# Kernel optimization log

Measured on AMD Instinct MI355X. Metric: run time of the kernel, lower is better.

Reference implementation:

```python
import math
import jax, jax.numpy as jnp
import numpy as np

B, LD, LS = 1, 512, 2048
C_S, C_H, H, PQ, PV = 384, 16, 12, 4, 8
EPS, INF = 1e-08, 1e9


def _quat_to_rot(q):
    q = q / jnp.linalg.norm(q, axis=-1, keepdims=True)
    w, x, y, z = q[..., 0], q[..., 1], q[..., 2], q[..., 3]
    R = jnp.stack([
        1 - 2 * (y * y + z * z), 2 * (x * y - w * z), 2 * (x * z + w * y),
        2 * (x * y + w * z), 1 - 2 * (x * x + z * z), 2 * (y * z - w * x),
        2 * (x * z - w * y), 2 * (y * z + w * x), 1 - 2 * (x * x + y * y)],
        axis=-1)
    return R.reshape(q.shape[:-1] + (3, 3))


def setup_inputs() -> dict:
    key = jax.random.key(0)
    ks = jax.random.split(key, 14)
    s_dst = jax.random.normal(ks[0], (B, LD, C_S), jnp.float32)
    s_src = jax.random.normal(ks[1], (B, LS, C_S), jnp.float32)
    R_dst = _quat_to_rot(jax.random.normal(ks[2], (B, LD, 4), jnp.float32))
    t_dst = jax.random.normal(ks[3], (B, LD, 3), jnp.float32) * 3.0
    R_src = _quat_to_rot(jax.random.normal(ks[4], (B, LS, 4), jnp.float32))
    t_src = jax.random.normal(ks[5], (B, LS, 3), jnp.float32) * 3.0
    dst_mask = jnp.ones((B, LD), jnp.float32)
    src_mask = (jax.random.uniform(ks[6], (B, LS)) < 0.9).astype(jnp.float32)
    sc = 0.02
    W_q = jax.random.normal(ks[7], (C_S, H * C_H), jnp.float32) * sc
    W_kv = jax.random.normal(ks[8], (C_S, 2 * H * C_H), jnp.float32) * sc
    W_qp = jax.random.normal(ks[9], (C_S, H * PQ * 3), jnp.float32) * sc
    W_kvp = jax.random.normal(ks[10], (C_S, H * (PQ + PV) * 3), jnp.float32) * sc
    W_out = jax.random.normal(ks[11], (H * (C_H + PV * 4), C_S), jnp.float32) * sc
    b_out = jnp.zeros((C_S,), jnp.float32)
    # ipa_point_weights_init_: softplus^-1(1) = log(e - 1)
    head_w = jnp.full((H,), float(np.log(np.e - 1.0)), jnp.float32)
    return dict(s_dst=s_dst, s_src=s_src, R_dst=R_dst, t_dst=t_dst,
                R_src=R_src, t_src=t_src, dst_mask=dst_mask, src_mask=src_mask,
                W_q=W_q, W_kv=W_kv, W_qp=W_qp, W_kvp=W_kvp,
                W_out=W_out, b_out=b_out, head_w=head_w)


def _split3_stack(x):
    # torch.split into 3 chunks on last dim then stack(dim=-1): [..., 3n] -> [..., n, 3]
    b, l, c3 = x.shape
    return jnp.moveaxis(x.reshape(b, l, 3, c3 // 3), -2, -1)


def _ipa_forward(s_dst, s_src, R_dst, t_dst, R_src, t_src, dst_mask, src_mask,
                 W_q, W_kv, W_qp, W_kvp, W_out, b_out, head_w):
    b, ld, _ = s_dst.shape
    ls = s_src.shape[1]
    gmask = (dst_mask[:, None, :, None] * src_mask[:, None, None, :])  # [B,1,Ld,Ls]

    q = (s_dst @ W_q).reshape(b, ld, H, C_H)
    kv = (s_src @ W_kv).reshape(b, ls, H, 2 * C_H)
    k, v = kv[..., :C_H], kv[..., C_H:]

    # points in global frame
    qp = _split3_stack(s_dst @ W_qp)                     # [B,Ld,H*PQ,3] local
    qp = jnp.einsum('blij,blpj->blpi', R_dst, qp) + t_dst[:, :, None, :]
    qp = qp.reshape(b, ld, H, PQ, 3)
    kvp = _split3_stack(s_src @ W_kvp)                   # [B,Ls,H*(PQ+PV),3]
    kvp = jnp.einsum('blij,blpj->blpi', R_src, kvp) + t_src[:, :, None, :]
    kvp = kvp.reshape(b, ls, H, PQ + PV, 3)
    k_pts, v_pts = kvp[..., :PQ, :], kvp[..., PQ:, :]

    # scalar attention scores
    a = jnp.einsum('bihc,bjhc->bhij', q, k) * math.sqrt(1.0 / (2 * C_H))
    a_sd = a * gmask

    # point attention: squared distances of global-frame points
    diff = qp[:, :, None, :, :, :] - k_pts[:, None, :, :, :, :]   # [B,Ld,Ls,H,PQ,3]
    pt2 = jnp.sum(diff * diff, axis=-1)                           # [B,Ld,Ls,H,PQ]
    hw = jax.nn.softplus(head_w) * math.sqrt(1.0 / (2 * (PQ * 9.0 / 2)))
    pt_att = jnp.sum(pt2 * hw[None, None, None, :, None], axis=-1) * (-0.5)
    pt_att = jnp.transpose(pt_att, (0, 3, 1, 2))                  # [B,H,Ld,Ls]
    a_pts = pt_att * gmask

    sq_mask = INF * (dst_mask[:, :, None] * src_mask[:, None, :] - 1.0)
    a = jax.nn.softmax(a + pt_att + sq_mask[:, None, :, :], axis=-1)

    # scalar value aggregation
    o = jnp.einsum('bhij,bjhc->bihc', a, v).reshape(b, ld, H * C_H)
    # point value aggregation, then back to dst local frame
    o_pt = jnp.einsum('bhij,bjhpc->bihpc', a, v_pts)              # [B,Ld,H,PV,3]
    o_pt = jnp.einsum('bikj,bihpk->bihpj', R_dst,
                      o_pt - t_dst[:, :, None, None, :])
    o_pt_norm = jnp.sqrt(jnp.sum(o_pt ** 2, axis=-1) + EPS).reshape(b, ld, H * PV)
    o_pt_flat = o_pt.reshape(b, ld, H * PV, 3)

    cat = jnp.concatenate([o, o_pt_flat[..., 0], o_pt_flat[..., 1],
                           o_pt_flat[..., 2], o_pt_norm], axis=-1)
    s_upd = cat @ W_out + b_out
    return s_upd, a, a_sd, a_pts


def reference(s_dst, s_src, R_dst, t_dst, R_src, t_src, dst_mask, src_mask,
              W_q, W_kv, W_qp, W_kvp, W_out, b_out, head_w):
    return _ipa_forward(s_dst, s_src, R_dst, t_dst, R_src, t_src,
                        dst_mask, src_mask, W_q, W_kv, W_qp, W_kvp,
                        W_out, b_out, head_w)
```

## Files before the change

### kernel.cpp

```cpp
#include <hip/hip_runtime.h>
#include <hip/hip_bf16.h>

#define LD 512
#define LS 2048
#define CS 384
#define CH 16
#define NH 12
#define PQ 4
#define PV 8
#define QCW 336
#define KVW 816

typedef __bf16 bf16x8 __attribute__((ext_vector_type(8)));
typedef float  f32x4  __attribute__((ext_vector_type(4)));

__device__ inline bf16x8 conv_frag(const float* __restrict__ p)
{
    float4 x = *(const float4*)p;
    float4 y = *(const float4*)(p + 4);
    bf16x8 h;
    h[0] = (__bf16)x.x; h[1] = (__bf16)x.y; h[2] = (__bf16)x.z; h[3] = (__bf16)x.w;
    h[4] = (__bf16)y.x; h[5] = (__bf16)y.y; h[6] = (__bf16)y.z; h[7] = (__bf16)y.w;
    return h;
}

__device__ inline bf16x8 conv_frag_w(const float* __restrict__ Wp, int stride)
{
    float f[8];
#pragma unroll
    for (int e = 0; e < 8; ++e) f[e] = Wp[(size_t)e * stride];
    bf16x8 h;
#pragma unroll
    for (int e = 0; e < 8; ++e) h[e] = (__bf16)f[e];
    return h;
}

__global__ __launch_bounds__(64) void proj_gemm_kernel(
    const float* __restrict__ s_dst, const float* __restrict__ s_src,
    const float* __restrict__ W_q, const float* __restrict__ W_qp,
    const float* __restrict__ W_kv, const float* __restrict__ W_kvp,
    float* __restrict__ qcat, float* __restrict__ kvcat)
{
    const float* A; float* C; int N, m0, n0, Nw; const float* Wsrc; int ncol0;
    if (blockIdx.x < 176) {
        int b = blockIdx.x;
        A = s_dst; C = qcat; N = QCW;
        m0 = (b & 15) * 32; n0 = (b >> 4) * 32;
        if (n0 < 192) { Wsrc = W_q;  Nw = 192; ncol0 = n0; }
        else          { Wsrc = W_qp; Nw = 144; ncol0 = n0 - 192; }
    } else {
        int b = blockIdx.x - 176;
        A = s_src; C = kvcat; N = KVW;
        m0 = (b & 63) * 32; n0 = (b >> 6) * 32;
        if (n0 < 384) { Wsrc = W_kv;  Nw = 384; ncol0 = n0; }
        else          { Wsrc = W_kvp; Nw = 432; ncol0 = n0 - 384; }
    }
    const int lane = threadIdx.x;
    const int row16 = lane & 15, kq = lane >> 4;
    const int K = CS;

    const float* ap0 = A + (size_t)(m0 + row16) * K + kq * 8;
    const float* ap1 = ap0 + (size_t)16 * K;
    const float* wp0 = Wsrc + (size_t)(kq * 8) * Nw + ncol0 + row16;
    const float* wp1 = wp0 + 16;
    const bool n1ok = (n0 + 16) < N;

    f32x4 acc00 = {0.f, 0.f, 0.f, 0.f};
    f32x4 acc10 = {0.f, 0.f, 0.f, 0.f};
    f32x4 acc01 = {0.f, 0.f, 0.f, 0.f};
    f32x4 acc11 = {0.f, 0.f, 0.f, 0.f};

    for (int k = 0; k < K; k += 32) {
        bf16x8 a0 = conv_frag(ap0 + k);
        bf16x8 a1 = conv_frag(ap1 + k);
        bf16x8 b0 = conv_frag_w(wp0 + (size_t)k * Nw, Nw);
        acc00 = __builtin_amdgcn_mfma_f32_16x16x32_bf16(a0, b0, acc00, 0, 0, 0);
        acc10 = __builtin_amdgcn_mfma_f32_16x16x32_bf16(a1, b0, acc10, 0, 0, 0);
        if (n1ok) {
            bf16x8 b1 = conv_frag_w(wp1 + (size_t)k * Nw, Nw);
            acc01 = __builtin_amdgcn_mfma_f32_16x16x32_bf16(a0, b1, acc01, 0, 0, 0);
            acc11 = __builtin_amdgcn_mfma_f32_16x16x32_bf16(a1, b1, acc11, 0, 0, 0);
        }
    }

#pragma unroll
    for (int r = 0; r < 4; ++r) {
        const int mA = m0 + kq * 4 + r;
        const int mB = mA + 16;
        C[(size_t)mA * N + n0 + row16] = acc00[r];
        C[(size_t)mB * N + n0 + row16] = acc10[r];
        if (n1ok) {
            C[(size_t)mA * N + n0 + 16 + row16] = acc01[r];
            C[(size_t)mB * N + n0 + 16 + row16] = acc11[r];
        }
    }
}

__global__ __launch_bounds__(256) void prep_kernel(
    const float* __restrict__ qcat, const float* __restrict__ kvcat,
    const float* __restrict__ Rd, const float* __restrict__ td,
    const float* __restrict__ Rs, const float* __restrict__ ts,
    float* __restrict__ qp_rot, float* __restrict__ sqq,
    float* __restrict__ kT, float* __restrict__ vAllT,
    float* __restrict__ kpT, float* __restrict__ sqkT)
{
    const int t = threadIdx.x;
    if (blockIdx.y < NH) {
        const int h = blockIdx.y, j0 = blockIdx.x * 64;
        __shared__ float tile[64][33];
        __shared__ float ot[36][64];
        __shared__ float nrm[64][4];
        __shared__ float rt[64][12];

#pragma unroll
        for (int s = 0; s < 3; ++s) {
            int ld = t + s * 256;
            int jl = ld / 12, q = ld % 12;
            rt[jl][q] = (q < 9) ? Rs[(size_t)(j0 + jl) * 9 + q]
                                : ts[(size_t)(j0 + jl) * 3 + (q - 9)];
        }
#pragma unroll
        for (int r = 0; r < 2; ++r) {
            int f = t + r * 256;
            int jl = f >> 3, c4 = (f & 7) * 4;
            float4 v = *(const float4*)(kvcat + (size_t)(j0 + jl) * KVW + h * 32 + c4);
            tile[jl][c4 + 0] = v.x;
            tile[jl][c4 + 1] = v.y;
            tile[jl][c4 + 2] = v.z;
            tile[jl][c4 + 3] = v.w;
        }
        __syncthreads();

        {
            const int jl = t & 63, cr = t >> 6;
#pragma unroll
            for (int cg = 0; cg < 8; ++cg) {
                int c = cg * 4 + cr;
                float v = tile[jl][c];
                if (c < 16) kT[((size_t)h * 16 + c) * LS + j0 + jl] = v;
                else        vAllT[((size_t)h * 40 + (c - 16)) * LS + j0 + jl] = v;
            }
        }

#pragma unroll
        for (int s = 0; s < 3; ++s) {
            int u = t + s * 256;
            int jl = u / 12, p = u % 12;
            const float* src = kvcat + (size_t)(j0 + jl) * KVW + 384 + h * 12 + p;
            float x = src[0], y = src[144], z = src[288];
            const float* R = &rt[jl][0];
            float rx = R[0] * x + R[1] * y + R[2] * z + R[9];
            float ry = R[3] * x + R[4] * y + R[5] * z + R[10];
            float rz = R[6] * x + R[7] * y + R[8] * z + R[11];
            if (p < 4) {
                ot[p * 3 + 0][jl] = rx;
                ot[p * 3 + 1][jl] = ry;
                ot[p * 3 + 2][jl] = rz;
                nrm[jl][p] = rx * rx + ry * ry + rz * rz;
            } else {
                int r0 = 12 + (p - 4) * 3;
                ot[r0 + 0][jl] = rx;
                ot[r0 + 1][jl] = ry;
                ot[r0 + 2][jl] = rz;
            }
        }
        __syncthreads();

#pragma unroll
        for (int w = 0; w < 9; ++w) {
            int idx = t + w * 256;
            int row = idx >> 6, jl = idx & 63;
            float v = ot[row][jl];
            if (row < 12) kpT[((size_t)h * 12 + row) * LS + j0 + jl] = v;
            else          vAllT[((size_t)h * 40 + 16 + (row - 12)) * LS + j0 + jl] = v;
        }
        if (t < 64)
            sqkT[(size_t)h * LS + j0 + t] = nrm[t][0] + nrm[t][1] + nrm[t][2] + nrm[t][3];
    } else {
        const int i0 = blockIdx.x * 16;
        __shared__ float part[16][48];
        __shared__ float rtd[16][12];
        if (t < 192) {
            int il = t / 12, q = t % 12;
            rtd[il][q] = (q < 9) ? Rd[(size_t)(i0 + il) * 9 + q]
                                 : td[(size_t)(i0 + il) * 3 + (q - 9)];
        }
        __syncthreads();
#pragma unroll
        for (int s = 0; s < 3; ++s) {
            int u = t + s * 256;
            int il = u / 48, pt = u % 48;
            int i = i0 + il;
            float x = qcat[(size_t)i * QCW + 192 + pt];
            float y = qcat[(size_t)i * QCW + 240 + pt];
            float z = qcat[(size_t)i * QCW + 288 + pt];
            const float* R = &rtd[il][0];
            float rx = R[0] * x + R[1] * y + R[2] * z + R[9];
            float ry = R[3] * x + R[4] * y + R[5] * z + R[10];
            float rz = R[6] * x + R[7] * y + R[8] * z + R[11];
            qp_rot[(size_t)i * 144 + pt * 3 + 0] = rx;
            qp_rot[(size_t)i * 144 + pt * 3 + 1] = ry;
            qp_rot[(size_t)i * 144 + pt * 3 + 2] = rz;
            part[il][pt] = rx * rx + ry * ry + rz * rz;
        }
        __syncthreads();
        if (t < 192) {
            int il = t / 12, hh = t % 12;
            sqq[(size_t)(i0 + il) * NH + hh] =
                part[il][hh * 4] + part[il][hh * 4 + 1] +
                part[il][hh * 4 + 2] + part[il][hh * 4 + 3];
        }
    }
}

__global__ __launch_bounds__(256) void score_softmax_kernel(
    const float* __restrict__ qb, const float* __restrict__ kT,
    const float* __restrict__ qpb, const float* __restrict__ kpT,
    const float* __restrict__ sqq_g, const float* __restrict__ sqkT,
    const float* __restrict__ dmask, const float* __restrict__ smask,
    const float* __restrict__ head_w,
    float* __restrict__ a_out, float* __restrict__ asd_out,
    float* __restrict__ apts_out)
{
    const int h = blockIdx.y;
    const int i0 = blockIdx.x * 4;
    const int t = threadIdx.x;

    __shared__ float qs[4][32];
    __shared__ float sqq_s[4];
    __shared__ float dm_s[4];
    __shared__ float red[4][4];

    if (t < 128) {
        int i = t >> 5, c = t & 31;
        float v = 0.f;
        if (c < 16)      v = qb[(size_t)(i0 + i) * QCW + h * CH + c];
        else if (c < 28) v = qpb[(size_t)(i0 + i) * 144 + h * 12 + (c - 16)];
        qs[i][c] = v;
    } else if (t < 132) {
        int i = t - 128;
        sqq_s[i] = sqq_g[(size_t)(i0 + i) * NH + h];
        dm_s[i] = dmask[i0 + i];
    }
    const float hwv = log1pf(__expf(head_w[h])) * (1.0f / 6.0f);
    const float s1 = 0.17677669529663687f;
    const size_t rowbase = ((size_t)h * LD + i0) * LS;
    __syncthreads();

    float4 sregv[4][2];
    float mx[4] = {-3.0e38f, -3.0e38f, -3.0e38f, -3.0e38f};

#pragma unroll
    for (int jc = 0; jc < 2; ++jc) {
        const int j = (jc * 256 + t) * 4;
        float4 sm4 = *(const float4*)(smask + j);
        float4 sqk4 = *(const float4*)(sqkT + (size_t)h * LS + j);

        float4 kk[16];
#pragma unroll
        for (int c = 0; c < 16; ++c)
            kk[c] = *(const float4*)(kT + ((size_t)h * 16 + c) * LS + j);

        float4 qk4[4];
#pragma unroll
        for (int i = 0; i < 4; ++i) {
            const float4* q4 = (const float4*)&qs[i][0];
            float4 q0 = q4[0], q1 = q4[1], q2 = q4[2], q3 = q4[3];
            float4 a;
            a.x = q0.x * kk[0].x + q0.y * kk[1].x + q0.z * kk[2].x + q0.w * kk[3].x
                + q1.x * kk[4].x + q1.y * kk[5].x + q1.z * kk[6].x + q1.w * kk[7].x
                + q2.x * kk[8].x + q2.y * kk[9].x + q2.z * kk[10].x + q2.w * kk[11].x
                + q3.x * kk[12].x + q3.y * kk[13].x + q3.z * kk[14].x + q3.w * kk[15].x;
            a.y = q0.x * kk[0].y + q0.y * kk[1].y + q0.z * kk[2].y + q0.w * kk[3].y
                + q1.x * kk[4].y + q1.y * kk[5].y + q1.z * kk[6].y + q1.w * kk[7].y
                + q2.x * kk[8].y + q2.y * kk[9].y + q2.z * kk[10].y + q2.w * kk[11].y
                + q3.x * kk[12].y + q3.y * kk[13].y + q3.z * kk[14].y + q3.w * kk[15].y;
            a.z = q0.x * kk[0].z + q0.y * kk[1].z + q0.z * kk[2].z + q0.w * kk[3].z
                + q1.x * kk[4].z + q1.y * kk[5].z + q1.z * kk[6].z + q1.w * kk[7].z
                + q2.x * kk[8].z + q2.y * kk[9].z + q2.z * kk[10].z + q2.w * kk[11].z
                + q3.x * kk[12].z + q3.y * kk[13].z + q3.z * kk[14].z + q3.w * kk[15].z;
            a.w = q0.x * kk[0].w + q0.y * kk[1].w + q0.z * kk[2].w + q0.w * kk[3].w
                + q1.x * kk[4].w + q1.y * kk[5].w + q1.z * kk[6].w + q1.w * kk[7].w
                + q2.x * kk[8].w + q2.y * kk[9].w + q2.z * kk[10].w + q2.w * kk[11].w
                + q3.x * kk[12].w + q3.y * kk[13].w + q3.z * kk[14].w + q3.w * kk[15].w;
            qk4[i] = a;
        }

        float4 pp[12];
#pragma unroll
        for (int d = 0; d < 12; ++d)
            pp[d] = *(const float4*)(kpT + ((size_t)h * 12 + d) * LS + j);

        float4 dp4[4];
#pragma unroll
        for (int i = 0; i < 4; ++i) {
            const float4* r4 = (const float4*)&qs[i][16];
            float4 r0 = r4[0], r1 = r4[1], r2 = r4[2];
            float4 d;
            d.x = r0.x * pp[0].x + r0.y * pp[1].x + r0.z * pp[2].x + r0.w * pp[3].x
                + r1.x * pp[4].x + r1.y * pp[5].x + r1.z * pp[6].x + r1.w * pp[7].x
                + r2.x * pp[8].x + r2.y * pp[9].x + r2.z * pp[10].x + r2.w * pp[11].x;
            d.y = r0.x * pp[0].y + r0.y * pp[1].y + r0.z * pp[2].y + r0.w * pp[3].y
                + r1.x * pp[4].y + r1.y * pp[5].y + r1.z * pp[6].y + r1.w * pp[7].y
                + r2.x * pp[8].y + r2.y * pp[9].y + r2.z * pp[10].y + r2.w * pp[11].y;
            d.z = r0.x * pp[0].z + r0.y * pp[1].z + r0.z * pp[2].z + r0.w * pp[3].z
                + r1.x * pp[4].z + r1.y * pp[5].z + r1.z * pp[6].z + r1.w * pp[7].z
                + r2.x * pp[8].z + r2.y * pp[9].z + r2.z * pp[10].z + r2.w * pp[11].z;
            d.w = r0.x * pp[0].w + r0.y * pp[1].w + r0.z * pp[2].w + r0.w * pp[3].w
                + r1.x * pp[4].w + r1.y * pp[5].w + r1.z * pp[6].w + r1.w * pp[7].w
                + r2.x * pp[8].w + r2.y * pp[9].w + r2.z * pp[10].w + r2.w * pp[11].w;
            dp4[i] = d;
        }

#pragma unroll
        for (int i = 0; i < 4; ++i) {
            float sqq = sqq_s[i];
            float dm = dm_s[i];
            float4 qk, pt, g, logit;
            qk.x = qk4[i].x * s1; qk.y = qk4[i].y * s1;
            qk.z = qk4[i].z * s1; qk.w = qk4[i].w * s1;
            pt.x = -0.5f * hwv * (sqq + sqk4.x - 2.f * dp4[i].x);
            pt.y = -0.5f * hwv * (sqq + sqk4.y - 2.f * dp4[i].y);
            pt.z = -0.5f * hwv * (sqq + sqk4.z - 2.f * dp4[i].z);
            pt.w = -0.5f * hwv * (sqq + sqk4.w - 2.f * dp4[i].w);
            g.x = dm * sm4.x; g.y = dm * sm4.y; g.z = dm * sm4.z; g.w = dm * sm4.w;
            size_t idx = rowbase + (size_t)i * LS + j;
            f32x4 asd = {qk.x * g.x, qk.y * g.y, qk.z * g.z, qk.w * g.w};
            f32x4 apts = {pt.x * g.x, pt.y * g.y, pt.z * g.z, pt.w * g.w};
            __builtin_nontemporal_store(asd, (f32x4*)(asd_out + idx));
            __builtin_nontemporal_store(apts, (f32x4*)(apts_out + idx));
            logit.x = qk.x + pt.x + 1.0e9f * (g.x - 1.0f);
            logit.y = qk.y + pt.y + 1.0e9f * (g.y - 1.0f);
            logit.z = qk.z + pt.z + 1.0e9f * (g.z - 1.0f);
            logit.w = qk.w + pt.w + 1.0e9f * (g.w - 1.0f);
            sregv[i][jc] = logit;
            mx[i] = fmaxf(mx[i], fmaxf(fmaxf(logit.x, logit.y), fmaxf(logit.z, logit.w)));
        }
    }

    const int lane = t & 63, wid = t >> 6;
#pragma unroll
    for (int i = 0; i < 4; ++i) {
        float v = mx[i];
        for (int off = 32; off > 0; off >>= 1) v = fmaxf(v, __shfl_xor(v, off));
        if (lane == 0) red[wid][i] = v;
    }
    __syncthreads();
    float M[4], sum[4] = {0.f, 0.f, 0.f, 0.f};
#pragma unroll
    for (int i = 0; i < 4; ++i)
        M[i] = fmaxf(fmaxf(red[0][i], red[1][i]), fmaxf(red[2][i], red[3][i]));
    __syncthreads();

#pragma unroll
    for (int jc = 0; jc < 2; ++jc) {
#pragma unroll
        for (int i = 0; i < 4; ++i) {
            float4 e;
            e.x = __expf(sregv[i][jc].x - M[i]);
            e.y = __expf(sregv[i][jc].y - M[i]);
            e.z = __expf(sregv[i][jc].z - M[i]);
            e.w = __expf(sregv[i][jc].w - M[i]);
            sregv[i][jc] = e;
            sum[i] += e.x + e.y + e.z + e.w;
        }
    }
#pragma unroll
    for (int i = 0; i < 4; ++i) {
        float v = sum[i];
        for (int off = 32; off > 0; off >>= 1) v += __shfl_xor(v, off);
        if (lane == 0) red[wid][i] = v;
    }
    __syncthreads();
    float inv[4];
#pragma unroll
    for (int i = 0; i < 4; ++i)
        inv[i] = 1.0f / (red[0][i] + red[1][i] + red[2][i] + red[3][i]);

#pragma unroll
    for (int jc = 0; jc < 2; ++jc) {
        const int j = (jc * 256 + t) * 4;
#pragma unroll
        for (int i = 0; i < 4; ++i) {
            float4 e = sregv[i][jc];
            float4 o = make_float4(e.x * inv[i], e.y * inv[i], e.z * inv[i], e.w * inv[i]);
            *(float4*)(a_out + rowbase + (size_t)i * LS + j) = o;
        }
    }
}

__global__ __launch_bounds__(512) void av_mfma_kernel(
    const float* __restrict__ a, const float* __restrict__ vAllT,
    float* __restrict__ o_buf, float* __restrict__ opt_buf)
{
    const int m0 = blockIdx.x * 16;
    const int h  = blockIdx.y;
    const int t = threadIdx.x;
    const int lane = t & 63;
    const int wid  = t >> 6;
    const int row16 = lane & 15, kq = lane >> 4;

    const size_t kbase = (size_t)wid * 256 + kq * 8;
    const float* ap  = a     + ((size_t)h * LD + m0 + row16) * LS + kbase;
    const float* v0p = vAllT + ((size_t)h * 40 +  0 + row16) * LS + kbase;
    const float* v1p = vAllT + ((size_t)h * 40 + 16 + row16) * LS + kbase;
    const float* v2p = vAllT + ((size_t)h * 40 + 24 + row16) * LS + kbase;

    f32x4 acc0 = {0.f, 0.f, 0.f, 0.f};
    f32x4 acc1 = {0.f, 0.f, 0.f, 0.f};
    f32x4 acc2 = {0.f, 0.f, 0.f, 0.f};

#pragma unroll 2
    for (int kk = 0; kk < 256; kk += 32) {
        bf16x8 ah = conv_frag(ap + kk);
        bf16x8 b0 = conv_frag(v0p + kk);
        bf16x8 b1 = conv_frag(v1p + kk);
        bf16x8 b2 = conv_frag(v2p + kk);
        acc0 = __builtin_amdgcn_mfma_f32_16x16x32_bf16(ah, b0, acc0, 0, 0, 0);
        acc1 = __builtin_amdgcn_mfma_f32_16x16x32_bf16(ah, b1, acc1, 0, 0, 0);
        acc2 = __builtin_amdgcn_mfma_f32_16x16x32_bf16(ah, b2, acc2, 0, 0, 0);
    }

    __shared__ float red[8][64][13];
#pragma unroll
    for (int r = 0; r < 4; ++r) {
        red[wid][lane][r]     = acc0[r];
        red[wid][lane][4 + r] = acc1[r];
        red[wid][lane][8 + r] = acc2[r];
    }
    __syncthreads();

    if (wid == 0) {
        float s[12];
#pragma unroll
        for (int r = 0; r < 12; ++r) {
            float v = red[0][lane][r];
#pragma unroll
            for (int w = 1; w < 8; ++w) v += red[w][lane][r];
            s[r] = v;
        }
        const int ib = m0 + kq * 4;
#pragma unroll
        for (int r = 0; r < 4; ++r) {
            const int i = ib + r;
            o_buf[(size_t)i * 192 + h * 16 + row16] = s[r];
            opt_buf[(size_t)i * 288 + h * 24 + row16] = s[4 + r];
            if (row16 >= 8)
                opt_buf[(size_t)i * 288 + h * 24 + 8 + row16] = s[8 + r];
        }
    }
}

__global__ __launch_bounds__(64) void finalize_out_kernel(
    const float* __restrict__ o_buf, const float* __restrict__ opt_buf,
    const float* __restrict__ Rd, const float* __restrict__ td,
    const float* __restrict__ W_out, const float* __restrict__ bias,
    float* __restrict__ out_s)
{
    const int m0 = blockIdx.x * 16;
    const int n0 = blockIdx.y * 32;
    const int t = threadIdx.x;

    __shared__ float cat[16][596];

    for (int u = t; u < 16 * 192; u += 64) {
        int il = u / 192, c = u % 192;
        cat[il][c] = o_buf[(size_t)(m0 + il) * 192 + c];
    }
    for (int u = t; u < 16 * 96; u += 64) {
        int il = u / 96, p = u % 96;
        int i = m0 + il;
        const float* op = opt_buf + (size_t)i * 288 + p * 3;
        float x = op[0] - td[i * 3 + 0];
        float y = op[1] - td[i * 3 + 1];
        float z = op[2] - td[i * 3 + 2];
        const float* R = Rd + i * 9;
        float rx = R[0] * x + R[3] * y + R[6] * z;
        float ry = R[1] * x + R[4] * y + R[7] * z;
        float rz = R[2] * x + R[5] * y + R[8] * z;
        cat[il][192 + p] = rx;
        cat[il][288 + p] = ry;
        cat[il][384 + p] = rz;
        cat[il][480 + p] = sqrtf(rx * rx + ry * ry + rz * rz + 1e-8f);
    }
    __syncthreads();

    const int row16 = t & 15, kq = t >> 4;
    f32x4 acc0 = {0.f, 0.f, 0.f, 0.f};
    f32x4 acc1 = {0.f, 0.f, 0.f, 0.f};

    for (int k = 0; k < 576; k += 32) {
        bf16x8 af = conv_frag(&cat[row16][k + kq * 8]);
        bf16x8 b0 = conv_frag_w(W_out + (size_t)(k + kq * 8) * CS + n0 + row16, CS);
        bf16x8 b1 = conv_frag_w(W_out + (size_t)(k + kq * 8) * CS + n0 + 16 + row16, CS);
        acc0 = __builtin_amdgcn_mfma_f32_16x16x32_bf16(af, b0, acc0, 0, 0, 0);
        acc1 = __builtin_amdgcn_mfma_f32_16x16x32_bf16(af, b1, acc1, 0, 0, 0);
    }

    const float bv0 = bias[n0 + row16];
    const float bv1 = bias[n0 + 16 + row16];
#pragma unroll
    for (int r = 0; r < 4; ++r) {
        const int m = m0 + kq * 4 + r;
        out_s[(size_t)m * CS + n0 + row16] = acc0[r] + bv0;
        out_s[(size_t)m * CS + n0 + 16 + row16] = acc1[r] + bv1;
    }
}

extern "C" void kernel_launch(void* const* d_in, const int* in_sizes, int n_in,
                              void* d_out, int out_size, void* d_ws, size_t ws_size,
                              hipStream_t stream)
{
    (void)in_sizes; (void)n_in; (void)out_size; (void)ws_size;
    const float* s_dst    = (const float*)d_in[0];
    const float* s_src    = (const float*)d_in[1];
    const float* R_dst    = (const float*)d_in[2];
    const float* t_dst    = (const float*)d_in[3];
    const float* R_src    = (const float*)d_in[4];
    const float* t_src    = (const float*)d_in[5];
    const float* dst_mask = (const float*)d_in[6];
    const float* src_mask = (const float*)d_in[7];
    const float* W_q      = (const float*)d_in[8];
    const float* W_kv     = (const float*)d_in[9];
    const float* W_qp     = (const float*)d_in[10];
    const float* W_kvp    = (const float*)d_in[11];
    const float* W_out    = (const float*)d_in[12];
    const float* b_out    = (const float*)d_in[13];
    const float* head_w   = (const float*)d_in[14];

    float* ws = (float*)d_ws;
    float* qcat    = ws;
    float* kvcat   = qcat    + 172032;
    float* qp_rot  = kvcat   + 1671168;
    float* sq_q    = qp_rot  + 73728;
    float* o_buf   = sq_q    + 6144;
    float* opt_buf = o_buf   + 98304;
    float* kT      = opt_buf + 147456;
    float* vAllT   = kT      + 393216;
    float* kpT     = vAllT   + 983040;
    float* sqkT    = kpT     + 294912;

    float* out_s    = (float*)d_out;
    float* out_a    = out_s    + 196608;
    float* out_asd  = out_a    + 12582912;
    float* out_apts = out_asd  + 12582912;

    proj_gemm_kernel<<<dim3(1840), dim3(64), 0, stream>>>(
        s_dst, s_src, W_q, W_qp, W_kv, W_kvp, qcat, kvcat);
    prep_kernel<<<dim3(32, 13), dim3(256), 0, stream>>>(
        qcat, kvcat, R_dst, t_dst, R_src, t_src,
        qp_rot, sq_q, kT, vAllT, kpT, sqkT);
    score_softmax_kernel<<<dim3(LD / 4, NH), dim3(256), 0, stream>>>(
        qcat, kT, qp_rot, kpT, sq_q, sqkT, dst_mask, src_mask, head_w,
        out_a, out_asd, out_apts);
    av_mfma_kernel<<<dim3(LD / 16, NH), dim3(512), 0, stream>>>(out_a, vAllT, o_buf, opt_buf);
    finalize_out_kernel<<<dim3(32, 12), dim3(64), 0, stream>>>(
        o_buf, opt_buf, R_dst, t_dst, W_out, b_out, out_s);
}
```

Measured before the change: 266.9 us.

## Stage projection weight tile in LDS and share across eight waves

The projection GEMM now runs 512-thread blocks, each covering 256 rows by 32 output columns. The block loads the 384x32 weight slice once into shared memory, transposed and padded, and every wave reads its B fragments from there. Before, each 64-thread block did strided global reads of the weights. This cuts redundant, uncoalesced weight traffic and launches far fewer blocks, at the cost of about 50KB of LDS per block and a block-wide sync before compute.

After: 273.7 us. 1.03x slower.

```diff
diff --git a/kernel.cpp b/kernel.cpp
--- a/kernel.cpp
+++ b/kernel.cpp
@@ -35,34 +35,47 @@
     return h;
 }
 
-__global__ __launch_bounds__(64) void proj_gemm_kernel(
+__global__ __launch_bounds__(512) void proj_gemm_kernel(
     const float* __restrict__ s_dst, const float* __restrict__ s_src,
     const float* __restrict__ W_q, const float* __restrict__ W_qp,
     const float* __restrict__ W_kv, const float* __restrict__ W_kvp,
     float* __restrict__ qcat, float* __restrict__ kvcat)
 {
-    const float* A; float* C; int N, m0, n0, Nw; const float* Wsrc; int ncol0;
-    if (blockIdx.x < 176) {
+    const float* A; float* C; int N, Nw, ncol0, n0, mbase; const float* Wsrc;
+    if (blockIdx.x < 22) {
         int b = blockIdx.x;
         A = s_dst; C = qcat; N = QCW;
-        m0 = (b & 15) * 32; n0 = (b >> 4) * 32;
+        int nt = b % 11, mg = b / 11;
+        n0 = nt * 32; mbase = mg * 256;
         if (n0 < 192) { Wsrc = W_q;  Nw = 192; ncol0 = n0; }
         else          { Wsrc = W_qp; Nw = 144; ncol0 = n0 - 192; }
     } else {
-        int b = blockIdx.x - 176;
+        int b = blockIdx.x - 22;
         A = s_src; C = kvcat; N = KVW;
-        m0 = (b & 63) * 32; n0 = (b >> 6) * 32;
+        int nt = b % 26, mg = b / 26;
+        n0 = nt * 32; mbase = mg * 256;
         if (n0 < 384) { Wsrc = W_kv;  Nw = 384; ncol0 = n0; }
         else          { Wsrc = W_kvp; Nw = 432; ncol0 = n0 - 384; }
     }
-    const int lane = threadIdx.x;
+
+    __shared__ float wlds[32][388];
+    const int t = threadIdx.x;
+
+#pragma unroll
+    for (int s = 0; s < 24; ++s) {
+        int idx = t + s * 512;
+        int k = idx >> 5, c = idx & 31;
+        float v = (ncol0 + c < Nw) ? Wsrc[(size_t)k * Nw + ncol0 + c] : 0.f;
+        wlds[c][k] = v;
+    }
+    __syncthreads();
+
+    const int lane = t & 63, wid = t >> 6;
     const int row16 = lane & 15, kq = lane >> 4;
-    const int K = CS;
-
-    const float* ap0 = A + (size_t)(m0 + row16) * K + kq * 8;
-    const float* ap1 = ap0 + (size_t)16 * K;
-    const float* wp0 = Wsrc + (size_t)(kq * 8) * Nw + ncol0 + row16;
-    const float* wp1 = wp0 + 16;
+    const int m0 = mbase + wid * 32;
+
+    const float* ap0 = A + (size_t)(m0 + row16) * CS + kq * 8;
+    const float* ap1 = ap0 + (size_t)16 * CS;
     const bool n1ok = (n0 + 16) < N;
 
     f32x4 acc00 = {0.f, 0.f, 0.f, 0.f};
@@ -70,14 +83,15 @@
     f32x4 acc01 = {0.f, 0.f, 0.f, 0.f};
     f32x4 acc11 = {0.f, 0.f, 0.f, 0.f};
 
-    for (int k = 0; k < K; k += 32) {
+#pragma unroll 4
+    for (int k = 0; k < CS; k += 32) {
         bf16x8 a0 = conv_frag(ap0 + k);
         bf16x8 a1 = conv_frag(ap1 + k);
-        bf16x8 b0 = conv_frag_w(wp0 + (size_t)k * Nw, Nw);
+        bf16x8 b0 = conv_frag(&wlds[row16][k + kq * 8]);
         acc00 = __builtin_amdgcn_mfma_f32_16x16x32_bf16(a0, b0, acc00, 0, 0, 0);
         acc10 = __builtin_amdgcn_mfma_f32_16x16x32_bf16(a1, b0, acc10, 0, 0, 0);
         if (n1ok) {
-            bf16x8 b1 = conv_frag_w(wp1 + (size_t)k * Nw, Nw);
+            bf16x8 b1 = conv_frag(&wlds[row16 + 16][k + kq * 8]);
             acc01 = __builtin_amdgcn_mfma_f32_16x16x32_bf16(a0, b1, acc01, 0, 0, 0);
             acc11 = __builtin_amdgcn_mfma_f32_16x16x32_bf16(a1, b1, acc11, 0, 0, 0);
         }
@@ -545,7 +559,7 @@
     float* out_asd  = out_a    + 12582912;
     float* out_apts = out_asd  + 12582912;
 
-    proj_gemm_kernel<<<dim3(1840), dim3(64), 0, stream>>>(
+    proj_gemm_kernel<<<dim3(230), dim3(512), 0, stream>>>(
         s_dst, s_src, W_q, W_qp, W_kv, W_kvp, qcat, kvcat);
     prep_kernel<<<dim3(32, 13), dim3(256), 0, stream>>>(
         qcat, kvcat, R_dst, t_dst, R_src, t_src,
```
